# Kernel tuning notes

Measured on AMD Instinct MI355X. Metric: run time of the kernel, lower is better.

The kernel has to match this reference:

```python
import jax, jax.numpy as jnp
import numpy as np

B, S, I, C, P = 64, 14, 32, 10, 4   # batch, spatial, in-caps/pos, classes, pose size
ROUTINGS = 3
EPS = 1e-9


def setup_inputs() -> dict:
    key = jax.random.key(0)
    k1, k2, k3, k4, k5 = jax.random.split(key, 5)
    return {
        "inputs_pose": jax.random.normal(k1, (B, S, S, I, P, P), jnp.float32),
        "inputs_activation": jax.random.uniform(k2, (B, S, S, I), jnp.float32),
        "w": jax.random.normal(k3, (1, I, C, P, P), jnp.float32),
        "beta_v": jax.random.normal(k4, (1, C), jnp.float32) * 0.1,
        "beta_a": jax.random.normal(k5, (1, C), jnp.float32) * 0.1,
    }


def _em_routing(votes, i_act, beta_v, beta_a, routings):
    # votes: [B, N, C, 16], i_act: [B, N]
    Bn, N, Cc, D = votes.shape
    rr = jnp.full((Bn, N, Cc, 1), 1.0 / Cc, votes.dtype)  # uniform init assignments
    bv = beta_v.reshape(1, 1, Cc, 1)
    ba = beta_a.reshape(1, 1, Cc, 1)
    it_min, it_max = 1.0, min(float(routings), 3.0)  # inverse-temperature schedule
    o_mean = o_act = None
    for it in range(routings):
        inv_temp = it_min + (it_max - it_min) * it / max(1.0, routings - 1.0)
        # --- M step ---
        rr_p = rr * i_act[:, :, None, None]                        # [B,N,C,1]
        rr_sum = jnp.sum(rr_p, axis=1, keepdims=True)              # [B,1,C,1]
        o_mean = jnp.sum(rr_p * votes, axis=1, keepdims=True) / rr_sum   # [B,1,C,16]
        o_var = jnp.sum(rr_p * jnp.square(votes - o_mean), axis=1, keepdims=True) / rr_sum
        o_stdv = jnp.sqrt(o_var)                                   # [B,1,C,16]
        cost = jnp.sum((bv + jnp.log(o_stdv + EPS)) * rr_sum, axis=-1, keepdims=True)  # [B,1,C,1]
        o_act = jax.nn.sigmoid(inv_temp * (ba - cost))             # [B,1,C,1]
        # --- E step (skipped on last iteration) ---
        if it < routings - 1:
            logp = (-jnp.sum(jnp.square(votes - o_mean) / (2.0 * jnp.square(o_stdv) + EPS),
                             axis=-1, keepdims=True)
                    - jnp.sum(jnp.log(o_stdv + EPS), axis=-1, keepdims=True))  # [B,N,C,1]
            zz = jnp.log(o_act + EPS) + logp
            rr = jax.nn.softmax(zz, axis=2)
    return o_mean[:, 0], o_act[:, 0, :, 0]  # [B,C,16], [B,C]


def reference(inputs_pose, inputs_activation, w, beta_v, beta_a):
    # mat_transform: votes[b,h,w,i,c] = pose[b,h,w,i] @ W[i,c]   (4x4 matmuls)
    votes = jnp.einsum('bhwipq,icqr->bhwicpr', inputs_pose, w[0])
    votes = votes.reshape(B, S, S, I, C, P * P)
    # coordinate addition: scaled (row+0.5)/S onto pose element 0, col onto element 1
    coord = (jnp.arange(S, dtype=votes.dtype) + 0.5) / S
    votes = votes.at[..., 0].add(coord[None, :, None, None, None])
    votes = votes.at[..., 1].add(coord[None, None, :, None, None])
    votes = votes.reshape(B, S * S * I, C, P * P)
    acts = inputs_activation.reshape(B, S * S * I)
    o_mean, o_act = _em_routing(votes, acts, beta_v, beta_a, ROUTINGS)
    pose = o_mean.reshape(B, C, P, P)
    return pose, o_act
```

## Files before the change

kernel.cpp:

```cpp
#include <hip/hip_runtime.h>
#include <math.h>

#define Bsz 64
#define Ssz 14
#define Isz 32
#define Csz 10
#define Dsz 16
#define Nsz (Ssz*Ssz*Isz)
#define EPSF 1e-9f

#define CH  640
#define NCH 10

__device__ __forceinline__ void compute_vote(const float* __restrict__ p,
                                             const float* __restrict__ Wi,
                                             float chh, float cww, float* v)
{
#pragma unroll
    for (int pr = 0; pr < 4; ++pr)
#pragma unroll
        for (int r = 0; r < 4; ++r)
            v[pr*4+r] = p[pr*4+0]*Wi[0*4+r] + p[pr*4+1]*Wi[1*4+r]
                      + p[pr*4+2]*Wi[2*4+r] + p[pr*4+3]*Wi[3*4+r];
    v[0] += chh;
    v[1] += cww;
}

__global__ __launch_bounds__(640) void m0_kernel(
    const float* __restrict__ pose,
    const float* __restrict__ act,
    const float* __restrict__ w,
    float* __restrict__ partials)
{
    const int b = blockIdx.x, chunk = blockIdx.y;
    const int tid = threadIdx.x, c = tid >> 6, lane = tid & 63;

    __shared__ float Wm[Csz][Isz*17];

    for (int t = tid; t < Csz*Isz*Dsz; t += 640) {
        int cc = t >> 9, rem = t & 511, i = rem >> 4, q = rem & 15;
        Wm[cc][i*17 + q] = w[(i*Csz + cc)*Dsz + q];
    }
    __syncthreads();

    float s0 = 0.f, s1[Dsz], s2[Dsz];
#pragma unroll
    for (int d = 0; d < Dsz; ++d) { s1[d] = 0.f; s2[d] = 0.f; }

    const float* poseb = pose + (size_t)b * Nsz * Dsz;
    const float* actb  = act  + (size_t)b * Nsz;
    const int base = chunk * CH;

    for (int nl = lane; nl < CH; nl += 64) {
        const int n = base + nl;
        if (n < Nsz) {
            const float4* pp = reinterpret_cast<const float4*>(poseb + (size_t)n * Dsz);
            float4 a0 = pp[0], a1 = pp[1], a2 = pp[2], a3 = pp[3];
            float p[16] = {a0.x,a0.y,a0.z,a0.w, a1.x,a1.y,a1.z,a1.w,
                           a2.x,a2.y,a2.z,a2.w, a3.x,a3.y,a3.z,a3.w};
            int i = n & 31, hw = n >> 5;
            int wc = hw % Ssz, hr = hw / Ssz;
            float wgt = actb[n] * (1.0f/Csz);
            float v[16];
            compute_vote(p, &Wm[c][i*17], (hr+0.5f)*(1.0f/Ssz), (wc+0.5f)*(1.0f/Ssz), v);
            s0 += wgt;
#pragma unroll
            for (int d = 0; d < Dsz; ++d) {
                float wv = wgt * v[d];
                s1[d] += wv;
                s2[d] += wv * v[d];
            }
        }
    }

#pragma unroll
    for (int m = 32; m >= 1; m >>= 1) {
        s0 += __shfl_xor(s0, m);
#pragma unroll
        for (int d = 0; d < Dsz; ++d) {
            s1[d] += __shfl_xor(s1[d], m);
            s2[d] += __shfl_xor(s2[d], m);
        }
    }
    if (lane == 0) {
        float* pt = partials + ((size_t)(b*Csz + c)*NCH + chunk)*33;
        pt[0] = s0;
#pragma unroll
        for (int d = 0; d < Dsz; ++d) { pt[1+d] = s1[d]; pt[17+d] = s2[d]; }
    }
}

__global__ __launch_bounds__(640) void em_kernel(
    const float* __restrict__ pose,
    const float* __restrict__ act,
    const float* __restrict__ w,
    const float* __restrict__ beta_v,
    const float* __restrict__ beta_a,
    const float* __restrict__ part_in,
    float* __restrict__ part_out,
    float inv_temp_prev)
{
    const int b = blockIdx.x, chunk = blockIdx.y;
    const int tid = threadIdx.x, wv = tid >> 6, lane = tid & 63;

    __shared__ float Wm[Csz][Isz*17];
    __shared__ float rr[Csz][CH];
    __shared__ float prm[Csz][33];
    __shared__ float Sv[Csz][33];
    __shared__ float lg[Csz][16];

    for (int t = tid; t < Csz*Isz*Dsz; t += 640) {
        int cc = t >> 9, rem = t & 511, i = rem >> 4, q = rem & 15;
        Wm[cc][i*17 + q] = w[(i*Csz + cc)*Dsz + q];
    }
    if (tid < Csz*33) {
        int c = tid / 33, j = tid - c*33;
        const float* pp = part_in + ((size_t)(b*Csz + c)*NCH)*33 + j;
        float s = 0.f;
        for (int ch2 = 0; ch2 < NCH; ++ch2) s += pp[ch2*33];
        Sv[c][j] = s;
    }
    __syncthreads();
    if (tid < Csz*Dsz) {
        int c = tid >> 4, d = tid & 15;
        float S0 = Sv[c][0];
        float mn  = Sv[c][1+d] / S0;
        float var = fmaxf(Sv[c][17+d] / S0 - mn*mn, 0.f);
        float stdv = sqrtf(var);
        prm[c][d]    = mn;
        prm[c][16+d] = 1.f / (2.f*var + EPSF);
        lg[c][d]     = __logf(stdv + EPSF);
    }
    __syncthreads();
    if (tid < Csz) {
        int c = tid;
        float sumlog = 0.f;
#pragma unroll
        for (int d = 0; d < Dsz; ++d) sumlog += lg[c][d];
        float cost = Sv[c][0] * (16.f * beta_v[c] + sumlog);
        float oact = 1.f / (1.f + __expf(-inv_temp_prev * (beta_a[c] - cost)));
        prm[c][32] = __logf(oact + EPSF) - sumlog;
    }
    __syncthreads();

    const int base = chunk * CH;
    const float* poseb = pose + (size_t)b * Nsz * Dsz;
    {
        const int n = base + tid;
        if (n < Nsz) {
            const float4* pp = reinterpret_cast<const float4*>(poseb + (size_t)n * Dsz);
            float4 a0 = pp[0], a1 = pp[1], a2 = pp[2], a3 = pp[3];
            float p[16] = {a0.x,a0.y,a0.z,a0.w, a1.x,a1.y,a1.z,a1.w,
                           a2.x,a2.y,a2.z,a2.w, a3.x,a3.y,a3.z,a3.w};
            int i = n & 31, hw = n >> 5;
            int wc = hw % Ssz, hr = hw / Ssz;
            float chh = (hr+0.5f)*(1.0f/Ssz), cww = (wc+0.5f)*(1.0f/Ssz);
            float a = act[(size_t)b*Nsz + n];

            float zz[Csz];
#pragma unroll
            for (int c = 0; c < Csz; ++c) {
                float v[16];
                compute_vote(p, &Wm[c][i*17], chh, cww, v);
                float quad = 0.f;
#pragma unroll
                for (int d = 0; d < Dsz; ++d) {
                    float dv = v[d] - prm[c][d];
                    quad += dv * dv * prm[c][16+d];
                }
                zz[c] = prm[c][32] - quad;
            }
            float zmax = zz[0];
#pragma unroll
            for (int c = 1; c < Csz; ++c) zmax = fmaxf(zmax, zz[c]);
            float zsum = 0.f;
#pragma unroll
            for (int c = 0; c < Csz; ++c) { zz[c] = __expf(zz[c] - zmax); zsum += zz[c]; }
            float sc = __fdividef(a, zsum);
#pragma unroll
            for (int c = 0; c < Csz; ++c) rr[c][tid] = zz[c] * sc;
        }
    }
    __syncthreads();

    const int c = wv;
    float s0 = 0.f, s1[Dsz], s2[Dsz];
#pragma unroll
    for (int d = 0; d < Dsz; ++d) { s1[d] = 0.f; s2[d] = 0.f; }

    for (int nl = lane; nl < CH; nl += 64) {
        const int n = base + nl;
        if (n < Nsz) {
            const float4* pp = reinterpret_cast<const float4*>(poseb + (size_t)n * Dsz);
            float4 a0 = pp[0], a1 = pp[1], a2 = pp[2], a3 = pp[3];
            float p[16] = {a0.x,a0.y,a0.z,a0.w, a1.x,a1.y,a1.z,a1.w,
                           a2.x,a2.y,a2.z,a2.w, a3.x,a3.y,a3.z,a3.w};
            int i = n & 31, hw = n >> 5;
            int wc = hw % Ssz, hr = hw / Ssz;
            float wgt = rr[c][nl];
            float v[16];
            compute_vote(p, &Wm[c][i*17], (hr+0.5f)*(1.0f/Ssz), (wc+0.5f)*(1.0f/Ssz), v);
            s0 += wgt;
#pragma unroll
            for (int d = 0; d < Dsz; ++d) {
                float wvv = wgt * v[d];
                s1[d] += wvv;
                s2[d] += wvv * v[d];
            }
        }
    }

#pragma unroll
    for (int m = 32; m >= 1; m >>= 1) {
        s0 += __shfl_xor(s0, m);
#pragma unroll
        for (int d = 0; d < Dsz; ++d) {
            s1[d] += __shfl_xor(s1[d], m);
            s2[d] += __shfl_xor(s2[d], m);
        }
    }
    if (lane == 0) {
        float* pt = part_out + ((size_t)(b*Csz + c)*NCH + chunk)*33;
        pt[0] = s0;
#pragma unroll
        for (int d = 0; d < Dsz; ++d) { pt[1+d] = s1[d]; pt[17+d] = s2[d]; }
    }
}

__global__ __launch_bounds__(64) void fin_kernel(
    const float* __restrict__ partials,
    const float* __restrict__ beta_v,
    const float* __restrict__ beta_a,
    float* __restrict__ out,
    float inv_temp)
{
    const int bc = blockIdx.x * 64 + threadIdx.x;
    if (bc >= Bsz*Csz) return;
    const int c = bc % Csz;

    float S[33];
#pragma unroll
    for (int j = 0; j < 33; ++j) S[j] = 0.f;
    const float* pb = partials + (size_t)bc * NCH * 33;
    for (int ch2 = 0; ch2 < NCH; ++ch2)
#pragma unroll
        for (int j = 0; j < 33; ++j) S[j] += pb[ch2*33 + j];

    float S0 = S[0], rS0 = 1.f / S0;
    float sumlog = 0.f;
    float* om = out + (size_t)bc * Dsz;
#pragma unroll
    for (int d = 0; d < Dsz; ++d) {
        float mn  = S[1+d] * rS0;
        float var = fmaxf(S[17+d] * rS0 - mn*mn, 0.f);
        sumlog += __logf(sqrtf(var) + EPSF);
        om[d] = mn;
    }
    float cost = S0 * (16.f * beta_v[c] + sumlog);
    float oact = 1.f / (1.f + __expf(-inv_temp * (beta_a[c] - cost)));
    out[Bsz*Csz*Dsz + bc] = oact;
}

extern "C" void kernel_launch(void* const* d_in, const int* in_sizes, int n_in,
                              void* d_out, int out_size, void* d_ws, size_t ws_size,
                              hipStream_t stream)
{
    const float* pose = (const float*)d_in[0];
    const float* act  = (const float*)d_in[1];
    const float* w    = (const float*)d_in[2];
    const float* bv   = (const float*)d_in[3];
    const float* ba   = (const float*)d_in[4];
    float* out = (float*)d_out;

    float* partA = (float*)d_ws;
    float* partB = partA + (size_t)Bsz*Csz*NCH*33;

    dim3 grid(Bsz, NCH);

    m0_kernel<<<grid, CH, 0, stream>>>(pose, act, w, partA);
    em_kernel<<<grid, CH, 0, stream>>>(pose, act, w, bv, ba, partA, partB, 1.0f);
    em_kernel<<<grid, CH, 0, stream>>>(pose, act, w, bv, ba, partB, partA, 2.0f);
    fin_kernel<<<(Bsz*Csz + 63)/64, 64, 0, stream>>>(partA, bv, ba, out, 3.0f);
}
```

Measured before the change: 226.2 us.

## Keep per-class W in registers and restructure E-step to class-per-wave layout

```diff
diff --git a/kernel.cpp b/kernel.cpp
--- a/kernel.cpp
+++ b/kernel.cpp
@@ -12,18 +12,38 @@
 #define CH  640
 #define NCH 10
 
-__device__ __forceinline__ void compute_vote(const float* __restrict__ p,
-                                             const float* __restrict__ Wi,
-                                             float chh, float cww, float* v)
+__device__ __forceinline__ void load_pose(const float* __restrict__ poseb, int n, float* p)
+{
+    const float4* pp = reinterpret_cast<const float4*>(poseb + (size_t)n * Dsz);
+    float4 a0 = pp[0], a1 = pp[1], a2 = pp[2], a3 = pp[3];
+    p[0]=a0.x; p[1]=a0.y; p[2]=a0.z; p[3]=a0.w;
+    p[4]=a1.x; p[5]=a1.y; p[6]=a1.z; p[7]=a1.w;
+    p[8]=a2.x; p[9]=a2.y; p[10]=a2.z; p[11]=a2.w;
+    p[12]=a3.x; p[13]=a3.y; p[14]=a3.z; p[15]=a3.w;
+}
+
+__device__ __forceinline__ void vote_reg(const float* p, const float* Wr,
+                                         float chh, float cww, float* v)
 {
 #pragma unroll
     for (int pr = 0; pr < 4; ++pr)
 #pragma unroll
         for (int r = 0; r < 4; ++r)
-            v[pr*4+r] = p[pr*4+0]*Wi[0*4+r] + p[pr*4+1]*Wi[1*4+r]
-                      + p[pr*4+2]*Wi[2*4+r] + p[pr*4+3]*Wi[3*4+r];
+            v[pr*4+r] = p[pr*4+0]*Wr[0*4+r] + p[pr*4+1]*Wr[1*4+r]
+                      + p[pr*4+2]*Wr[2*4+r] + p[pr*4+3]*Wr[3*4+r];
     v[0] += chh;
     v[1] += cww;
+}
+
+__device__ __forceinline__ void load_W_regs(const float* __restrict__ w,
+                                            int lane, int c, float* Wr)
+{
+    const float4* ws = reinterpret_cast<const float4*>(w + (((lane & 31)*Csz + c) * Dsz));
+    float4 b0 = ws[0], b1 = ws[1], b2 = ws[2], b3 = ws[3];
+    Wr[0]=b0.x; Wr[1]=b0.y; Wr[2]=b0.z; Wr[3]=b0.w;
+    Wr[4]=b1.x; Wr[5]=b1.y; Wr[6]=b1.z; Wr[7]=b1.w;
+    Wr[8]=b2.x; Wr[9]=b2.y; Wr[10]=b2.z; Wr[11]=b2.w;
+    Wr[12]=b3.x; Wr[13]=b3.y; Wr[14]=b3.z; Wr[15]=b3.w;
 }
 
 __global__ __launch_bounds__(640) void m0_kernel(
@@ -35,13 +55,8 @@
     const int b = blockIdx.x, chunk = blockIdx.y;
     const int tid = threadIdx.x, c = tid >> 6, lane = tid & 63;
 
-    __shared__ float Wm[Csz][Isz*17];
-
-    for (int t = tid; t < Csz*Isz*Dsz; t += 640) {
-        int cc = t >> 9, rem = t & 511, i = rem >> 4, q = rem & 15;
-        Wm[cc][i*17 + q] = w[(i*Csz + cc)*Dsz + q];
-    }
-    __syncthreads();
+    float Wr[16];
+    load_W_regs(w, lane, c, Wr);
 
     float s0 = 0.f, s1[Dsz], s2[Dsz];
 #pragma unroll
@@ -54,15 +69,13 @@
     for (int nl = lane; nl < CH; nl += 64) {
         const int n = base + nl;
         if (n < Nsz) {
-            const float4* pp = reinterpret_cast<const float4*>(poseb + (size_t)n * Dsz);
-            float4 a0 = pp[0], a1 = pp[1], a2 = pp[2], a3 = pp[3];
-            float p[16] = {a0.x,a0.y,a0.z,a0.w, a1.x,a1.y,a1.z,a1.w,
-                           a2.x,a2.y,a2.z,a2.w, a3.x,a3.y,a3.z,a3.w};
-            int i = n & 31, hw = n >> 5;
+            float p[16];
+            load_pose(poseb, n, p);
+            int hw = n >> 5;
             int wc = hw % Ssz, hr = hw / Ssz;
             float wgt = actb[n] * (1.0f/Csz);
             float v[16];
-            compute_vote(p, &Wm[c][i*17], (hr+0.5f)*(1.0f/Ssz), (wc+0.5f)*(1.0f/Ssz), v);
+            vote_reg(p, Wr, (hr+0.5f)*(1.0f/Ssz), (wc+0.5f)*(1.0f/Ssz), v);
             s0 += wgt;
 #pragma unroll
             for (int d = 0; d < Dsz; ++d) {
@@ -103,16 +116,14 @@
     const int b = blockIdx.x, chunk = blockIdx.y;
     const int tid = threadIdx.x, wv = tid >> 6, lane = tid & 63;
 
-    __shared__ float Wm[Csz][Isz*17];
-    __shared__ float rr[Csz][CH];
+    __shared__ float zz[CH][11];
+    __shared__ float Sv[Csz][33];
     __shared__ float prm[Csz][33];
-    __shared__ float Sv[Csz][33];
     __shared__ float lg[Csz][16];
 
-    for (int t = tid; t < Csz*Isz*Dsz; t += 640) {
-        int cc = t >> 9, rem = t & 511, i = rem >> 4, q = rem & 15;
-        Wm[cc][i*17 + q] = w[(i*Csz + cc)*Dsz + q];
-    }
+    float Wr[16];
+    load_W_regs(w, lane, wv, Wr);
+
     if (tid < Csz*33) {
         int c = tid / 33, j = tid - c*33;
         const float* pp = part_in + ((size_t)(b*Csz + c)*NCH)*33 + j;
@@ -126,10 +137,9 @@
         float S0 = Sv[c][0];
         float mn  = Sv[c][1+d] / S0;
         float var = fmaxf(Sv[c][17+d] / S0 - mn*mn, 0.f);
-        float stdv = sqrtf(var);
         prm[c][d]    = mn;
         prm[c][16+d] = 1.f / (2.f*var + EPSF);
-        lg[c][d]     = __logf(stdv + EPSF);
+        lg[c][d]     = __logf(sqrtf(var) + EPSF);
     }
     __syncthreads();
     if (tid < Csz) {
@@ -145,45 +155,53 @@
 
     const int base = chunk * CH;
     const float* poseb = pose + (size_t)b * Nsz * Dsz;
+
+    {
+        float mn[Dsz], iv[Dsz];
+#pragma unroll
+        for (int d = 0; d < Dsz; ++d) { mn[d] = prm[wv][d]; iv[d] = prm[wv][16+d]; }
+        float Kc = prm[wv][32];
+
+        for (int nl = lane; nl < CH; nl += 64) {
+            const int n = base + nl;
+            if (n < Nsz) {
+                float p[16];
+                load_pose(poseb, n, p);
+                int hw = n >> 5;
+                int wc = hw % Ssz, hr = hw / Ssz;
+                float v[16];
+                vote_reg(p, Wr, (hr+0.5f)*(1.0f/Ssz), (wc+0.5f)*(1.0f/Ssz), v);
+                float quad = 0.f;
+#pragma unroll
+                for (int d = 0; d < Dsz; ++d) {
+                    float dv = v[d] - mn[d];
+                    quad += dv * dv * iv[d];
+                }
+                zz[nl][wv] = Kc - quad;
+            }
+        }
+    }
+    __syncthreads();
+
     {
         const int n = base + tid;
         if (n < Nsz) {
-            const float4* pp = reinterpret_cast<const float4*>(poseb + (size_t)n * Dsz);
-            float4 a0 = pp[0], a1 = pp[1], a2 = pp[2], a3 = pp[3];
-            float p[16] = {a0.x,a0.y,a0.z,a0.w, a1.x,a1.y,a1.z,a1.w,
-                           a2.x,a2.y,a2.z,a2.w, a3.x,a3.y,a3.z,a3.w};
-            int i = n & 31, hw = n >> 5;
-            int wc = hw % Ssz, hr = hw / Ssz;
-            float chh = (hr+0.5f)*(1.0f/Ssz), cww = (wc+0.5f)*(1.0f/Ssz);
-            float a = act[(size_t)b*Nsz + n];
-
-            float zz[Csz];
-#pragma unroll
-            for (int c = 0; c < Csz; ++c) {
-                float v[16];
-                compute_vote(p, &Wm[c][i*17], chh, cww, v);
-                float quad = 0.f;
-#pragma unroll
-                for (int d = 0; d < Dsz; ++d) {
-                    float dv = v[d] - prm[c][d];
-                    quad += dv * dv * prm[c][16+d];
-                }
-                zz[c] = prm[c][32] - quad;
-            }
-            float zmax = zz[0];
-#pragma unroll
-            for (int c = 1; c < Csz; ++c) zmax = fmaxf(zmax, zz[c]);
+            float z[Csz];
+#pragma unroll
+            for (int c = 0; c < Csz; ++c) z[c] = zz[tid][c];
+            float zmax = z[0];
+#pragma unroll
+            for (int c = 1; c < Csz; ++c) zmax = fmaxf(zmax, z[c]);
             float zsum = 0.f;
 #pragma unroll
-            for (int c = 0; c < Csz; ++c) { zz[c] = __expf(zz[c] - zmax); zsum += zz[c]; }
-            float sc = __fdividef(a, zsum);
-#pragma unroll
-            for (int c = 0; c < Csz; ++c) rr[c][tid] = zz[c] * sc;
-        }
-    }
-    __syncthreads();
-
-    const int c = wv;
+            for (int c = 0; c < Csz; ++c) { z[c] = __expf(z[c] - zmax); zsum += z[c]; }
+            float sc = __fdividef(act[(size_t)b*Nsz + n], zsum);
+#pragma unroll
+            for (int c = 0; c < Csz; ++c) zz[tid][c] = z[c] * sc;
+        }
+    }
+    __syncthreads();
+
     float s0 = 0.f, s1[Dsz], s2[Dsz];
 #pragma unroll
     for (int d = 0; d < Dsz; ++d) { s1[d] = 0.f; s2[d] = 0.f; }
@@ -191,15 +209,13 @@
     for (int nl = lane; nl < CH; nl += 64) {
         const int n = base + nl;
         if (n < Nsz) {
-            const float4* pp = reinterpret_cast<const float4*>(poseb + (size_t)n * Dsz);
-            float4 a0 = pp[0], a1 = pp[1], a2 = pp[2], a3 = pp[3];
-            float p[16] = {a0.x,a0.y,a0.z,a0.w, a1.x,a1.y,a1.z,a1.w,
-                           a2.x,a2.y,a2.z,a2.w, a3.x,a3.y,a3.z,a3.w};
-            int i = n & 31, hw = n >> 5;
+            float p[16];
+            load_pose(poseb, n, p);
+            int hw = n >> 5;
             int wc = hw % Ssz, hr = hw / Ssz;
-            float wgt = rr[c][nl];
+            float wgt = zz[nl][wv];
             float v[16];
-            compute_vote(p, &Wm[c][i*17], (hr+0.5f)*(1.0f/Ssz), (wc+0.5f)*(1.0f/Ssz), v);
+            vote_reg(p, Wr, (hr+0.5f)*(1.0f/Ssz), (wc+0.5f)*(1.0f/Ssz), v);
             s0 += wgt;
 #pragma unroll
             for (int d = 0; d < Dsz; ++d) {
@@ -220,7 +236,7 @@
         }
     }
     if (lane == 0) {
-        float* pt = part_out + ((size_t)(b*Csz + c)*NCH + chunk)*33;
+        float* pt = part_out + ((size_t)(b*Csz + wv)*NCH + chunk)*33;
         pt[0] = s0;
 #pragma unroll
         for (int d = 0; d < Dsz; ++d) { pt[1+d] = s1[d]; pt[17+d] = s2[d]; }
```

After: 233.2 us. +3.1%, slower.
